# Kernel optimization log

Measured on AMD Instinct MI355X. Metric: run time of the kernel, lower is better.

## Reference

```python
import jax, jax.numpy as jnp
import numpy as np

B = 8192      # batch
LAT = 256     # latent_dimension
HID = 512     # hidden_size
INP = 128     # input_size (n_layer_types + 1 feature)
T = 64        # max_length
MLP = 512     # fixed MLP width in source


def _lin(key, fan_in, fan_out):
    kw, kb = jax.random.split(key)
    s = 1.0 / np.sqrt(fan_in)
    W = jax.random.uniform(kw, (fan_in, fan_out), jnp.float32, -s, s)
    b = jax.random.uniform(kb, (fan_out,), jnp.float32, -s, s)
    return W, b


def setup_inputs() -> dict:
    key = jax.random.key(0)
    ks = jax.random.split(key, 16)
    x = jax.random.normal(ks[0], (B, LAT), jnp.float32)
    W1, b1 = _lin(ks[1], LAT, MLP)
    W2, b2 = _lin(ks[2], MLP, MLP)
    W3, b3 = _lin(ks[3], MLP, MLP)
    Wh1, bh1 = _lin(ks[4], MLP, MLP)
    Wh2, bh2 = _lin(ks[5], MLP, HID)
    Wc1, bc1 = _lin(ks[6], MLP, MLP)
    Wc2, bc2 = _lin(ks[7], MLP, HID)
    Wx1, bx1 = _lin(ks[8], MLP, MLP)
    Wx2, bx2 = _lin(ks[9], MLP, INP)
    Wih, bih = _lin(ks[10], INP, 4 * HID)   # LSTM input->gates (i,f,g,o)
    Whh, bhh = _lin(ks[11], HID, 4 * HID)   # LSTM hidden->gates
    Wp, bp = _lin(ks[12], HID, INP)          # predictor head
    return dict(x=x, W1=W1, b1=b1, W2=W2, b2=b2, W3=W3, b3=b3,
                Wh1=Wh1, bh1=bh1, Wh2=Wh2, bh2=bh2,
                Wc1=Wc1, bc1=bc1, Wc2=Wc2, bc2=bc2,
                Wx1=Wx1, bx1=bx1, Wx2=Wx2, bx2=bx2,
                Wih=Wih, bih=bih, Whh=Whh, bhh=bhh, Wp=Wp, bp=bp)


def _lrelu(v):
    return jnp.where(v >= 0, v, 0.2 * v)


def _head(v):
    # split [d-1, 1]: softmax over layer types, sigmoid on feature scalar
    lt = jax.nn.softmax(v[..., :-1], axis=-1)
    ft = jax.nn.sigmoid(v[..., -1:])
    return jnp.concatenate([lt, ft], axis=-1)


def reference(x, W1, b1, W2, b2, W3, b3, Wh1, bh1, Wh2, bh2,
              Wc1, bc1, Wc2, bc2, Wx1, bx1, Wx2, bx2,
              Wih, bih, Whh, bhh, Wp, bp):
    z = _lrelu(x @ W1 + b1)
    z = _lrelu(z @ W2 + b2)
    z = _lrelu(z @ W3 + b3)
    h = _lrelu(z @ Wh1 + bh1) @ Wh2 + bh2          # [B, HID]
    c = _lrelu(z @ Wc1 + bc1) @ Wc2 + bc2          # [B, HID]
    x0 = _head(_lrelu(z @ Wx1 + bx1) @ Wx2 + bx2)  # [B, INP]

    def step(carry, _):
        xt, h, c = carry
        g = xt @ Wih + h @ Whh + (bih + bhh)        # [B, 4*HID]
        i, f, gg, o = jnp.split(g, 4, axis=-1)      # torch gate order i,f,g,o
        c2 = jax.nn.sigmoid(f) * c + jax.nn.sigmoid(i) * jnp.tanh(gg)
        h2 = jax.nn.sigmoid(o) * jnp.tanh(c2)
        nxt = _head(h2 @ Wp + bp)
        return (nxt, h2, c2), nxt

    # The torch loop reruns the LSTM over the growing prefix with the same
    # initial (h,c) and takes the last output; by LSTM causality this equals
    _, ys = jax.lax.scan(step, (x0, h, c), None, length=T)
    return jnp.transpose(ys, (1, 0, 2))  # [B, T, INP]
```

## Files before the change

### kernel.cpp

```cpp
#include <hip/hip_runtime.h>


typedef _Float16 h16;
typedef __attribute__((ext_vector_type(8))) _Float16 f16x8;
typedef __attribute__((ext_vector_type(4))) float f32x4;

#define BB 8192
#define TT 64

__device__ __forceinline__ void gload16(const void* g, void* lds) {
  __builtin_amdgcn_global_load_lds(
      (const __attribute__((address_space(1))) unsigned int*)g,
      (__attribute__((address_space(3))) unsigned int*)lds, 16, 0, 0);
}

__device__ __forceinline__ float sigm(float x) { return 1.f / (1.f + __expf(-x)); }
__device__ __forceinline__ float tanhf_(float x) { return 2.f / (1.f + __expf(-2.f * x)) - 1.f; }

#define MIDBAR_LG()                                        \
  do {                                                     \
    __builtin_amdgcn_s_barrier();                          \
    asm volatile("s_waitcnt lgkmcnt(0)" ::: "memory");     \
    __builtin_amdgcn_sched_barrier(0);                     \
  } while (0)
#define ENDBAR()                                           \
  do {                                                     \
    __builtin_amdgcn_s_barrier();                          \
    asm volatile("" ::: "memory");                         \
  } while (0)

__global__ __launch_bounds__(512, 2) void gate4(
    const h16* __restrict__ A, const h16* __restrict__ Bt,
    const float* __restrict__ bg, float* __restrict__ Cbuf,
    h16* __restrict__ Hout) {
  __shared__ __align__(16) h16 As[2][16384];
  __shared__ __align__(16) h16 Bs[2][16384];
  const int tid = threadIdx.x;
  const int lane = tid & 63;
  const int wid = tid >> 6;
  const int wr = wid >> 2, wc = wid & 3;
  const int m0 = blockIdx.x * 256;
  const int n0 = blockIdx.y * 256;
  const int arow = lane & 15, khi = lane >> 4;
  const int x7 = arow & 7;

  auto stage = [&](h16(*dst)[16384], int slot, int h, const h16* src, int base,
                   int kt) {
#pragma unroll
    for (int li = 0; li < 2; ++li) {
      int rowbase = li * 128 + h * 64 + wid * 8;
      int row = rowbase + (lane >> 3);
      int gc = (lane & 7) ^ (lane >> 3);
      gload16(src + (size_t)(base + row) * 640 + kt * 64 + gc * 8,
              &dst[slot][rowbase * 64]);
    }
  };

  f32x4 acc[8][4];
#pragma unroll
  for (int i = 0; i < 8; ++i)
#pragma unroll
    for (int jj = 0; jj < 4; ++jj) acc[i][jj] = (f32x4)0.f;
  f16x8 af[2][4], bf[2][4];

  auto readA2 = [&](int slot, int ms) {
#pragma unroll
    for (int ks = 0; ks < 2; ++ks)
#pragma unroll
      for (int mr = 0; mr < 4; ++mr) {
        int r = wr * 128 + ms * 64 + mr * 16 + arow;
        af[ks][mr] = *(const f16x8*)&As[slot][r * 64 + ((ks * 4 + khi) ^ x7) * 8];
      }
  };
  auto readB = [&](int slot, int ks) {
#pragma unroll
    for (int jj = 0; jj < 4; ++jj) {
      int rb = wc * 64 + jj * 16 + arow;
      bf[ks][jj] = *(const f16x8*)&Bs[slot][rb * 64 + ((ks * 4 + khi) ^ x7) * 8];
    }
  };
  auto mfma32 = [&](int ms) {
    __builtin_amdgcn_s_setprio(1);
#pragma unroll
    for (int ks = 0; ks < 2; ++ks)
#pragma unroll
      for (int mr = 0; mr < 4; ++mr)
#pragma unroll
        for (int jj = 0; jj < 4; ++jj)
          acc[ms * 4 + mr][jj] = __builtin_amdgcn_mfma_f32_16x16x32_f16(
              af[ks][mr], bf[ks][jj], acc[ms * 4 + mr][jj], 0, 0, 0);
    __builtin_amdgcn_s_setprio(0);
  };

  stage(Bs, 0, 0, Bt, n0, 0);
  stage(Bs, 0, 1, Bt, n0, 0);
  stage(As, 0, 0, A, m0, 0);
  stage(As, 0, 1, A, m0, 0);
  stage(Bs, 1, 0, Bt, n0, 1);
  stage(Bs, 1, 1, Bt, n0, 1);
  stage(As, 1, 0, A, m0, 1);
  asm volatile("s_waitcnt vmcnt(6)" ::: "memory");
  ENDBAR();

#pragma unroll 1
  for (int i = 0; i < 5; ++i) {
    const int t2 = 2 * i + 2, t3 = 2 * i + 3;
    readB(0, 0);
    readB(0, 1);
    readA2(0, 0);
    stage(As, 1, 1, A, m0, 2 * i + 1);
    if (t2 < 10) stage(Bs, 0, 0, Bt, n0, t2);
    MIDBAR_LG();
    mfma32(0);
    ENDBAR();
    readA2(0, 1);
    if (t2 < 10) {
      stage(Bs, 0, 1, Bt, n0, t2);
      stage(As, 0, 0, A, m0, t2);
    }
    if (i < 4)
      asm volatile("s_waitcnt vmcnt(6)" ::: "memory");
    else
      asm volatile("s_waitcnt vmcnt(0)" ::: "memory");
    MIDBAR_LG();
    mfma32(1);
    ENDBAR();
    readB(1, 0);
    readB(1, 1);
    readA2(1, 0);
    if (t2 < 10) stage(As, 0, 1, A, m0, t2);
    if (t3 < 10) stage(Bs, 1, 0, Bt, n0, t3);
    MIDBAR_LG();
    mfma32(0);
    ENDBAR();
    readA2(1, 1);
    if (t3 < 10) {
      stage(Bs, 1, 1, Bt, n0, t3);
      stage(As, 1, 0, A, m0, t3);
    }
    if (i < 4)
      asm volatile("s_waitcnt vmcnt(6)" ::: "memory");
    else
      asm volatile("s_waitcnt vmcnt(0)" ::: "memory");
    MIDBAR_LG();
    mfma32(1);
    ENDBAR();
  }

  const int nb = n0 + wc * 64;
  const float bI = bg[nb + arow];
  const float bF = bg[nb + 16 + arow];
  const float bG = bg[nb + 32 + arow];
  const float bO = bg[nb + 48 + arow];
  const int hj = blockIdx.y * 64 + wc * 16 + arow;
#pragma unroll
  for (int mrep = 0; mrep < 8; ++mrep) {
#pragma unroll
    for (int r = 0; r < 4; ++r) {
      int m = m0 + wr * 128 + mrep * 16 + khi * 4 + r;
      float gi = sigm(acc[mrep][0][r] + bI);
      float gf = sigm(acc[mrep][1][r] + bF);
      float gg = tanhf_(acc[mrep][2][r] + bG);
      float go = sigm(acc[mrep][3][r] + bO);
      size_t ci = (size_t)m * 512 + hj;
      float c2 = gf * Cbuf[ci] + gi * gg;
      Cbuf[ci] = c2;
      Hout[(size_t)m * 640 + 128 + hj] = (h16)(go * tanhf_(c2));
    }
  }
}

__global__ __launch_bounds__(256) void head256(
    const h16* __restrict__ A, int lda, const h16* __restrict__ Bt,
    const float* __restrict__ bias, int nkt, h16* __restrict__ Xout,
    float* __restrict__ ydst, int tstep, int swz) {
  __shared__ __align__(16) h16 As[2][32 * 64];
  __shared__ __align__(16) h16 Bs[2][128 * 64];
  __shared__ float lgs[32 * 132];
  const int tid = threadIdx.x;
  const int lane = tid & 63;
  const int w = tid >> 6;
  const int rs = w & 1, ch = w >> 1;
  const int arow = lane & 15, khi = lane >> 4;
  const int x7 = arow & 7;

  int bid = blockIdx.x;
  int m0;
  if (swz) {
    int g = bid & 7, k = bid >> 3;
    m0 = (g + 8 * (k & 3)) * 256 + (k >> 2) * 32;
  } else {
    m0 = bid * 32;
  }

  auto stageA = [&](int slot, int kt) {
    int rowbase = w * 8;
    int gc = (lane & 7) ^ (lane >> 3);
    int row = rowbase + (lane >> 3);
    gload16(A + (size_t)(m0 + row) * lda + kt * 64 + gc * 8,
            &As[slot][rowbase * 64]);
  };
  auto stageB = [&](int slot, int kt) {
#pragma unroll
    for (int li = 0; li < 4; ++li) {
      int rowbase = li * 32 + w * 8;
      int row = rowbase + (lane >> 3);
      int gc = (lane & 7) ^ (lane >> 3);
      gload16(Bt + (size_t)row * 512 + kt * 64 + gc * 8, &Bs[slot][rowbase * 64]);
    }
  };

  f32x4 acc[4];
#pragma unroll
  for (int j = 0; j < 4; ++j) acc[j] = (f32x4)0.f;

  stageA(0, 0);
  stageB(0, 0);
#pragma unroll 1
  for (int kt = 0; kt < nkt; ++kt) {
    int p = kt & 1;
    if (kt + 1 < nkt) {
      stageA(p ^ 1, kt + 1);
      stageB(p ^ 1, kt + 1);
      asm volatile("s_waitcnt vmcnt(5)" ::: "memory");
    } else {
      asm volatile("s_waitcnt vmcnt(0)" ::: "memory");
    }
    ENDBAR();
#pragma unroll
    for (int kk = 0; kk < 2; ++kk) {
      int kc = kk * 4 + khi;
      int ra = rs * 16 + arow;
      f16x8 afr = *(const f16x8*)&As[p][ra * 64 + (kc ^ x7) * 8];
#pragma unroll
      for (int j = 0; j < 4; ++j) {
        int rb = (ch * 4 + j) * 16 + arow;
        f16x8 bfr = *(const f16x8*)&Bs[p][rb * 64 + (kc ^ x7) * 8];
        acc[j] = __builtin_amdgcn_mfma_f32_16x16x32_f16(afr, bfr, acc[j], 0, 0, 0);
      }
    }
    ENDBAR();
  }

#pragma unroll
  for (int j = 0; j < 4; ++j)
#pragma unroll
    for (int r = 0; r < 4; ++r)
      lgs[(rs * 16 + khi * 4 + r) * 132 + (ch * 4 + j) * 16 + arow] = acc[j][r];
  __syncthreads();
  {
    int row = tid >> 3, g8 = tid & 7;
    float v[16];
    float mx = -1e30f;
#pragma unroll
    for (int q = 0; q < 16; ++q) {
      int col = g8 * 16 + q;
      v[q] = lgs[row * 132 + col] + bias[col];
      if (col != 127) mx = fmaxf(mx, v[q]);
    }
#pragma unroll
    for (int s = 1; s < 8; s <<= 1) mx = fmaxf(mx, __shfl_xor(mx, s, 8));
    float sm = 0.f;
#pragma unroll
    for (int q = 0; q < 16; ++q) {
      int col = g8 * 16 + q;
      if (col != 127) sm += __expf(v[q] - mx);
    }
#pragma unroll
    for (int s = 1; s < 8; s <<= 1) sm += __shfl_xor(sm, s, 8);
    float inv = 1.f / sm;
    h16 xo[16];
    float yo[16];
#pragma unroll
    for (int q = 0; q < 16; ++q) {
      int col = g8 * 16 + q;
      float res = (col == 127) ? sigm(v[q]) : __expf(v[q] - mx) * inv;
      xo[q] = (h16)res;
      yo[q] = res;
    }
    h16* xd = Xout + (size_t)(m0 + row) * 640 + g8 * 16;
    *(f16x8*)xd = *(f16x8*)&xo[0];
    *(f16x8*)(xd + 8) = *(f16x8*)&xo[8];
    if (ydst) {
      float* yd = ydst + ((size_t)(m0 + row) * 64 + tstep) * 128 + g8 * 16;
#pragma unroll
      for (int q = 0; q < 4; ++q) *(f32x4*)(yd + 4 * q) = *(f32x4*)&yo[4 * q];
    }
  }
}

enum { EP_LRELU = 0, EP_LIN16 = 1, EP_F32 = 2 };

template <int EP>
__global__ __launch_bounds__(256) void gemm128(
    const h16* __restrict__ A, int lda, const h16* __restrict__ Bt,
    const float* __restrict__ bias, int K, h16* __restrict__ out16, int ldo,
    int ocol, float* __restrict__ outf, int ldf) {
  __shared__ __align__(16) h16 As[128 * 64];
  __shared__ __align__(16) h16 Bs[128 * 64];
  const int tid = threadIdx.x;
  const int lane = tid & 63;
  const int w = tid >> 6;
  const int m0 = blockIdx.x * 128;
  const int n0 = blockIdx.y * 128;

  f32x4 acc[4][4];
#pragma unroll
  for (int i = 0; i < 4; ++i)
#pragma unroll
    for (int jj = 0; jj < 4; ++jj) acc[i][jj] = (f32x4)0.f;

  const int rh = (w >> 1) * 64;
  const int arow = lane & 15;
  const int khi = lane >> 4;

  const int nkt = K >> 6;
  for (int kt = 0; kt < nkt; ++kt) {
#pragma unroll
    for (int li = 0; li < 4; ++li) {
      int L = w * 4 + li;
      int r = L * 8 + (lane >> 3);
      int c = lane & 7;
      int gc = c ^ (r & 7);
      gload16(A + (size_t)(m0 + r) * lda + kt * 64 + gc * 8, &As[L * 512]);
      gload16(Bt + (size_t)(n0 + r) * K + kt * 64 + gc * 8, &Bs[L * 512]);
    }
    __syncthreads();
#pragma unroll
    for (int kk = 0; kk < 2; ++kk) {
      const int kc = kk * 4 + khi;
      f16x8 af[4], bf[4];
#pragma unroll
      for (int mt = 0; mt < 4; ++mt) {
        int r = rh + mt * 16 + arow;
        af[mt] = *(const f16x8*)&As[r * 64 + (kc ^ (r & 7)) * 8];
      }
#pragma unroll
      for (int jj = 0; jj < 4; ++jj) {
        int nt = (w & 1) * 4 + jj;
        int r = nt * 16 + arow;
        bf[jj] = *(const f16x8*)&Bs[r * 64 + (kc ^ (r & 7)) * 8];
      }
#pragma unroll
      for (int mt = 0; mt < 4; ++mt)
#pragma unroll
        for (int jj = 0; jj < 4; ++jj)
          acc[mt][jj] =
              __builtin_amdgcn_mfma_f32_16x16x32_f16(af[mt], bf[jj], acc[mt][jj], 0, 0, 0);
    }
    __syncthreads();
  }

#pragma unroll
  for (int mt = 0; mt < 4; ++mt) {
#pragma unroll
    for (int jj = 0; jj < 4; ++jj) {
      int nt = (w & 1) * 4 + jj;
      int n = n0 + nt * 16 + arow;
      float bv = bias[n];
#pragma unroll
      for (int r = 0; r < 4; ++r) {
        int m = m0 + rh + mt * 16 + khi * 4 + r;
        float v = acc[mt][jj][r] + bv;
        if constexpr (EP == EP_LRELU) {
          v = v >= 0.f ? v : 0.2f * v;
          out16[(size_t)m * ldo + n] = (h16)v;
        } else if constexpr (EP == EP_LIN16) {
          out16[(size_t)m * ldo + ocol + n] = (h16)v;
        } else {
          outf[(size_t)m * ldf + n] = v;
        }
      }
    }
  }
}

__global__ void cvt16(const float* __restrict__ in, h16* __restrict__ out, int n) {
  int i = blockIdx.x * 256 + threadIdx.x;
  if (i < n) out[i] = (h16)in[i];
}

__global__ void transposeW(const float* __restrict__ W, h16* __restrict__ WT, int K,
                           int N) {
  int i = blockIdx.x * 256 + threadIdx.x;
  if (i >= K * N) return;
  int k = i / N, n = i % N;
  WT[(size_t)n * K + k] = (h16)W[i];
}

__global__ void prep_gate(const float* __restrict__ Wih, const float* __restrict__ Whh,
                          const float* __restrict__ bih, const float* __restrict__ bhh,
                          h16* __restrict__ WgT, float* __restrict__ bg) {
  int i = blockIdx.x * 256 + threadIdx.x;
  if (i >= 2048 * 640) return;
  int np = i / 640, k = i % 640;
  int by = np >> 8, wcc = (np >> 6) & 3, q = (np >> 4) & 3, jj = np & 15;
  int orig = q * 512 + by * 64 + wcc * 16 + jj;
  float wv = (k < 128) ? Wih[(size_t)k * 2048 + orig]
                       : Whh[(size_t)(k - 128) * 2048 + orig];
  WgT[i] = (h16)wv;
  if (k == 0) bg[np] = bih[orig] + bhh[orig];
}

extern "C" void kernel_launch(void* const* d_in, const int* in_sizes, int n_in,
                              void* d_out, int out_size, void* d_ws, size_t ws_size,
                              hipStream_t stream) {
  const float* x = (const float*)d_in[0];
  const float* W1 = (const float*)d_in[1];
  const float* b1 = (const float*)d_in[2];
  const float* W2 = (const float*)d_in[3];
  const float* b2 = (const float*)d_in[4];
  const float* W3 = (const float*)d_in[5];
  const float* b3 = (const float*)d_in[6];
  const float* Wh1 = (const float*)d_in[7];
  const float* bh1 = (const float*)d_in[8];
  const float* Wh2 = (const float*)d_in[9];
  const float* bh2 = (const float*)d_in[10];
  const float* Wc1 = (const float*)d_in[11];
  const float* bc1 = (const float*)d_in[12];
  const float* Wc2 = (const float*)d_in[13];
  const float* bc2 = (const float*)d_in[14];
  const float* Wx1 = (const float*)d_in[15];
  const float* bx1 = (const float*)d_in[16];
  const float* Wx2 = (const float*)d_in[17];
  const float* bx2 = (const float*)d_in[18];
  const float* Wih = (const float*)d_in[19];
  const float* bih = (const float*)d_in[20];
  const float* Whh = (const float*)d_in[21];
  const float* bhh = (const float*)d_in[22];
  const float* Wp = (const float*)d_in[23];
  const float* bp = (const float*)d_in[24];

  char* ws = (char*)d_ws;
  size_t off = 0;
  auto take = [&](size_t bytes) -> void* {
    void* p = ws + off;
    off += (bytes + 255) & ~(size_t)255;
    return p;
  };
  h16* X16 = (h16*)take((size_t)BB * 256 * 2);
  h16* Za = (h16*)take((size_t)BB * 512 * 2);
  h16* Zb = (h16*)take((size_t)BB * 512 * 2);
  h16* XHa = (h16*)take((size_t)BB * 640 * 2);
  h16* XHb = (h16*)take((size_t)BB * 640 * 2);
  float* C = (float*)take((size_t)BB * 512 * 4);
  h16* W1T = (h16*)take(256 * 512 * 2);
  h16* W2T = (h16*)take(512 * 512 * 2);
  h16* W3T = (h16*)take(512 * 512 * 2);
  h16* Wh1T = (h16*)take(512 * 512 * 2);
  h16* Wh2T = (h16*)take(512 * 512 * 2);
  h16* Wc1T = (h16*)take(512 * 512 * 2);
  h16* Wc2T = (h16*)take(512 * 512 * 2);
  h16* Wx1T = (h16*)take(512 * 512 * 2);
  h16* Wx2T = (h16*)take(128 * 512 * 2);
  h16* WpT = (h16*)take(128 * 512 * 2);
  h16* WgT = (h16*)take((size_t)2048 * 640 * 2);
  float* bg = (float*)take(2048 * 4);

  dim3 blk(256);
  cvt16<<<(BB * 256 + 255) / 256, blk, 0, stream>>>(x, X16, BB * 256);
  transposeW<<<(256 * 512 + 255) / 256, blk, 0, stream>>>(W1, W1T, 256, 512);
  transposeW<<<(512 * 512 + 255) / 256, blk, 0, stream>>>(W2, W2T, 512, 512);
  transposeW<<<(512 * 512 + 255) / 256, blk, 0, stream>>>(W3, W3T, 512, 512);
  transposeW<<<(512 * 512 + 255) / 256, blk, 0, stream>>>(Wh1, Wh1T, 512, 512);
  transposeW<<<(512 * 512 + 255) / 256, blk, 0, stream>>>(Wh2, Wh2T, 512, 512);
  transposeW<<<(512 * 512 + 255) / 256, blk, 0, stream>>>(Wc1, Wc1T, 512, 512);
  transposeW<<<(512 * 512 + 255) / 256, blk, 0, stream>>>(Wc2, Wc2T, 512, 512);
  transposeW<<<(512 * 512 + 255) / 256, blk, 0, stream>>>(Wx1, Wx1T, 512, 512);
  transposeW<<<(512 * 128 + 255) / 256, blk, 0, stream>>>(Wx2, Wx2T, 512, 128);
  transposeW<<<(512 * 128 + 255) / 256, blk, 0, stream>>>(Wp, WpT, 512, 128);
  prep_gate<<<(2048 * 640 + 255) / 256, blk, 0, stream>>>(Wih, Whh, bih, bhh, WgT, bg);

  gemm128<EP_LRELU><<<dim3(64, 4), blk, 0, stream>>>(X16, 256, W1T, b1, 256, Za, 512, 0, nullptr, 0);
  gemm128<EP_LRELU><<<dim3(64, 4), blk, 0, stream>>>(Za, 512, W2T, b2, 512, Zb, 512, 0, nullptr, 0);
  gemm128<EP_LRELU><<<dim3(64, 4), blk, 0, stream>>>(Zb, 512, W3T, b3, 512, Za, 512, 0, nullptr, 0);
  gemm128<EP_LRELU><<<dim3(64, 4), blk, 0, stream>>>(Za, 512, Wh1T, bh1, 512, Zb, 512, 0, nullptr, 0);
  gemm128<EP_LIN16><<<dim3(64, 4), blk, 0, stream>>>(Zb, 512, Wh2T, bh2, 512, XHa, 640, 128, nullptr, 0);
  gemm128<EP_LRELU><<<dim3(64, 4), blk, 0, stream>>>(Za, 512, Wc1T, bc1, 512, Zb, 512, 0, nullptr, 0);
  gemm128<EP_F32><<<dim3(64, 4), blk, 0, stream>>>(Zb, 512, Wc2T, bc2, 512, nullptr, 0, 0, C, 512);
  gemm128<EP_LRELU><<<dim3(64, 4), blk, 0, stream>>>(Za, 512, Wx1T, bx1, 512, Zb, 512, 0, nullptr, 0);
  head256<<<256, blk, 0, stream>>>(Zb, 512, Wx2T, bx2, 8, XHa, nullptr, 0, 0);

  float* yout = (float*)d_out;
  for (int t = 0; t < TT; ++t) {
    h16* in_ = (t & 1) ? XHb : XHa;
    h16* out_ = (t & 1) ? XHa : XHb;
    gate4<<<dim3(32, 8), dim3(512), 0, stream>>>(in_, WgT, bg, C, out_);
    head256<<<256, blk, 0, stream>>>(out_ + 128, 640, WpT, bp, 8, out_, yout, t, 1);
  }
}
```

Before: 2.744 ms.

## Restructure LSTM gate GEMM pipeline into two phases per K-tile

The gate GEMM main loop moves from a four-phase-per-two-tiles schedule, where A/B fragment reads and partial MFMA batches were interleaved with staggered global-to-LDS loads, to a simpler two-phase schedule. Each phase reads every fragment for one K-tile into registers, issues the whole next tile's loads, then runs all 64 MFMAs. This cuts the number of barriers per tile. It costs more fragment registers (af doubles), which could hurt occupancy at 2 blocks per CU, and the load issue is less finely interleaved.

```diff
diff --git a/kernel.cpp b/kernel.cpp
--- a/kernel.cpp
+++ b/kernel.cpp
@@ -29,7 +29,7 @@
     asm volatile("" ::: "memory");                         \
   } while (0)
 
-__global__ __launch_bounds__(512, 2) void gate4(
+__global__ __launch_bounds__(512, 2) void gate2(
     const h16* __restrict__ A, const h16* __restrict__ Bt,
     const float* __restrict__ bg, float* __restrict__ Cbuf,
     h16* __restrict__ Hout) {
@@ -55,95 +55,79 @@
               &dst[slot][rowbase * 64]);
     }
   };
+  auto stageTile = [&](int slot, int kt) {
+    stage(Bs, slot, 0, Bt, n0, kt);
+    stage(Bs, slot, 1, Bt, n0, kt);
+    stage(As, slot, 0, A, m0, kt);
+    stage(As, slot, 1, A, m0, kt);
+  };
 
   f32x4 acc[8][4];
 #pragma unroll
   for (int i = 0; i < 8; ++i)
 #pragma unroll
     for (int jj = 0; jj < 4; ++jj) acc[i][jj] = (f32x4)0.f;
-  f16x8 af[2][4], bf[2][4];
-
-  auto readA2 = [&](int slot, int ms) {
+  f16x8 af[2][2][4];
+  f16x8 bf[2][4];
+
+  auto readAll = [&](int slot) {
 #pragma unroll
     for (int ks = 0; ks < 2; ++ks)
 #pragma unroll
-      for (int mr = 0; mr < 4; ++mr) {
-        int r = wr * 128 + ms * 64 + mr * 16 + arow;
-        af[ks][mr] = *(const f16x8*)&As[slot][r * 64 + ((ks * 4 + khi) ^ x7) * 8];
+      for (int jj = 0; jj < 4; ++jj) {
+        int rb = wc * 64 + jj * 16 + arow;
+        bf[ks][jj] = *(const f16x8*)&Bs[slot][rb * 64 + ((ks * 4 + khi) ^ x7) * 8];
       }
-  };
-  auto readB = [&](int slot, int ks) {
-#pragma unroll
-    for (int jj = 0; jj < 4; ++jj) {
-      int rb = wc * 64 + jj * 16 + arow;
-      bf[ks][jj] = *(const f16x8*)&Bs[slot][rb * 64 + ((ks * 4 + khi) ^ x7) * 8];
-    }
-  };
-  auto mfma32 = [&](int ms) {
+#pragma unroll
+    for (int ms = 0; ms < 2; ++ms)
+#pragma unroll
+      for (int ks = 0; ks < 2; ++ks)
+#pragma unroll
+        for (int mr = 0; mr < 4; ++mr) {
+          int r = wr * 128 + ms * 64 + mr * 16 + arow;
+          af[ms][ks][mr] =
+              *(const f16x8*)&As[slot][r * 64 + ((ks * 4 + khi) ^ x7) * 8];
+        }
+  };
+  auto mfma64 = [&]() {
     __builtin_amdgcn_s_setprio(1);
 #pragma unroll
-    for (int ks = 0; ks < 2; ++ks)
-#pragma unroll
-      for (int mr = 0; mr < 4; ++mr)
-#pragma unroll
-        for (int jj = 0; jj < 4; ++jj)
-          acc[ms * 4 + mr][jj] = __builtin_amdgcn_mfma_f32_16x16x32_f16(
-              af[ks][mr], bf[ks][jj], acc[ms * 4 + mr][jj], 0, 0, 0);
+    for (int ms = 0; ms < 2; ++ms)
+#pragma unroll
+      for (int ks = 0; ks < 2; ++ks)
+#pragma unroll
+        for (int mr = 0; mr < 4; ++mr)
+#pragma unroll
+          for (int jj = 0; jj < 4; ++jj)
+            acc[ms * 4 + mr][jj] = __builtin_amdgcn_mfma_f32_16x16x32_f16(
+                af[ms][ks][mr], bf[ks][jj], acc[ms * 4 + mr][jj], 0, 0, 0);
     __builtin_amdgcn_s_setprio(0);
   };
 
-  stage(Bs, 0, 0, Bt, n0, 0);
-  stage(Bs, 0, 1, Bt, n0, 0);
-  stage(As, 0, 0, A, m0, 0);
-  stage(As, 0, 1, A, m0, 0);
-  stage(Bs, 1, 0, Bt, n0, 1);
-  stage(Bs, 1, 1, Bt, n0, 1);
-  stage(As, 1, 0, A, m0, 1);
-  asm volatile("s_waitcnt vmcnt(6)" ::: "memory");
+  stageTile(0, 0);
+  stageTile(1, 1);
+  asm volatile("s_waitcnt vmcnt(8)" ::: "memory");
   ENDBAR();
 
 #pragma unroll 1
   for (int i = 0; i < 5; ++i) {
-    const int t2 = 2 * i + 2, t3 = 2 * i + 3;
-    readB(0, 0);
-    readB(0, 1);
-    readA2(0, 0);
-    stage(As, 1, 1, A, m0, 2 * i + 1);
-    if (t2 < 10) stage(Bs, 0, 0, Bt, n0, t2);
+    readAll(0);
     MIDBAR_LG();
-    mfma32(0);
-    ENDBAR();
-    readA2(0, 1);
-    if (t2 < 10) {
-      stage(Bs, 0, 1, Bt, n0, t2);
-      stage(As, 0, 0, A, m0, t2);
-    }
+    if (i < 4) stageTile(0, 2 * i + 2);
+    mfma64();
     if (i < 4)
-      asm volatile("s_waitcnt vmcnt(6)" ::: "memory");
+      asm volatile("s_waitcnt vmcnt(8)" ::: "memory");
     else
       asm volatile("s_waitcnt vmcnt(0)" ::: "memory");
+    ENDBAR();
+    readAll(1);
     MIDBAR_LG();
-    mfma32(1);
-    ENDBAR();
-    readB(1, 0);
-    readB(1, 1);
-    readA2(1, 0);
-    if (t2 < 10) stage(As, 0, 1, A, m0, t2);
-    if (t3 < 10) stage(Bs, 1, 0, Bt, n0, t3);
-    MIDBAR_LG();
-    mfma32(0);
-    ENDBAR();
-    readA2(1, 1);
-    if (t3 < 10) {
-      stage(Bs, 1, 1, Bt, n0, t3);
-      stage(As, 1, 0, A, m0, t3);
-    }
+    if (i < 4) stageTile(1, 2 * i + 3);
+    mfma64();
     if (i < 4)
-      asm volatile("s_waitcnt vmcnt(6)" ::: "memory");
+      asm volatile("s_waitcnt vmcnt(8)" ::: "memory");
     else
       asm volatile("s_waitcnt vmcnt(0)" ::: "memory");
-    MIDBAR_LG();
-    mfma32(1);
     ENDBAR();
   }
 
@@ -485,7 +469,7 @@
   for (int t = 0; t < TT; ++t) {
     h16* in_ = (t & 1) ? XHb : XHa;
     h16* out_ = (t & 1) ? XHa : XHb;
-    gate4<<<dim3(32, 8), dim3(512), 0, stream>>>(in_, WgT, bg, C, out_);
+    gate2<<<dim3(32, 8), dim3(512), 0, stream>>>(in_, WgT, bg, C, out_);
     head256<<<256, blk, 0, stream>>>(out_ + 128, 640, WpT, bp, 8, out_, yout, t, 1);
   }
 }
```

After: 4.954 ms. +80.5%, slower.
